# Optimization experiments

Measured on AMD Instinct MI355X. Metric: run time of the kernel, lower is better.

Reference implementation:

```python
import jax, jax.numpy as jnp
import numpy as np

IOU_THRESH = 0.5


def _conv(x, w, b):
    y = jax.lax.conv_general_dilated(
        x, w, window_strides=(1, 1), padding='SAME',
        dimension_numbers=('NCHW', 'OIHW', 'NCHW'))
    return jax.nn.relu(y + b[None, :, None, None])


def _nms_keep(boxes):
    # boxes: [N,4] xyxy, sorted by descending score. Returns bool keep mask [N].
    x1, y1, x2, y2 = boxes[:, 0], boxes[:, 1], boxes[:, 2], boxes[:, 3]
    area = jnp.maximum(x2 - x1, 0.0) * jnp.maximum(y2 - y1, 0.0)
    xx1 = jnp.maximum(x1[:, None], x1[None, :])
    yy1 = jnp.maximum(y1[:, None], y1[None, :])
    xx2 = jnp.minimum(x2[:, None], x2[None, :])
    yy2 = jnp.minimum(y2[:, None], y2[None, :])
    inter = jnp.maximum(xx2 - xx1, 0.0) * jnp.maximum(yy2 - yy1, 0.0)
    iou = inter / (area[:, None] + area[None, :] - inter + 1e-9)  # [N,N]
    n = boxes.shape[0]
    idx = jnp.arange(n)

    def body(i, keep):
        # suppress later boxes that overlap box i too much, if i itself is kept
        suppress = (iou[i] > IOU_THRESH) & (idx > i) & keep[i]
        return keep & ~suppress

    return jax.lax.fori_loop(0, n, body, jnp.ones((n,), dtype=bool))


def setup_inputs() -> dict:
    key = jax.random.key(0)
    k = jax.random.split(key, 7)
    B, N = 32, 100
    x = jax.random.normal(k[0], (B, 3, 224, 224), dtype=jnp.float32)
    boxes = jax.random.uniform(k[1], (B, N, 4), dtype=jnp.float32) * 224.0
    scores = jax.random.uniform(k[2], (B, N), dtype=jnp.float32)
    w1 = jax.random.normal(k[3], (64, 3, 3, 3), dtype=jnp.float32) * (1.0 / np.sqrt(3 * 9))
    b1 = jnp.zeros((64,), dtype=jnp.float32)
    w2 = jax.random.normal(k[4], (128, 64, 3, 3), dtype=jnp.float32) * (1.0 / np.sqrt(64 * 9))
    b2 = jnp.zeros((128,), dtype=jnp.float32)
    return {'x': x, 'boxes': boxes, 'scores': scores,
            'w1': w1, 'b1': b1, 'w2': w2, 'b2': b2}


def reference(x, boxes, scores, w1, b1, w2, b2):
    # backbone: conv-relu-conv-relu-globalavgpool-flatten -> [B,128]
    h = _conv(x, w1, b1)
    h = _conv(h, w2, b2)
    feats = jnp.mean(h, axis=(2, 3))  # AdaptiveAvgPool2d((1,1)) + Flatten

    # per-image sort by descending score
    order = jnp.argsort(-scores, axis=1)                         # [B,N]
    boxes_sorted = jnp.take_along_axis(boxes, order[..., None], axis=1)
    scores_sorted = jnp.take_along_axis(scores, order, axis=1)

    # batched greedy NMS; fixed-shape keep mask instead of ragged index lists
    keep = jax.vmap(_nms_keep)(boxes_sorted)                     # [B,N] bool

    final_boxes = jnp.where(keep[..., None], boxes_sorted, 0.0)
    final_scores = jnp.where(keep, scores_sorted, 0.0)
    return feats, final_boxes, final_scores, keep
```

## Files before the change

### kernel.cpp

```cpp
#include <hip/hip_runtime.h>
#include <hip/hip_bf16.h>

#define HH 224
#define WW 224

#define OUT_FEATS  0
#define OUT_BOXES  4096
#define OUT_SCORES 16896
#define OUT_KEEP   20096

typedef __attribute__((ext_vector_type(8))) short short8;
typedef __attribute__((ext_vector_type(4))) float f32x4;
typedef __attribute__((ext_vector_type(4))) unsigned int u32x4;
typedef __attribute__((ext_vector_type(2))) unsigned int u32x2;

static __device__ __forceinline__ unsigned short f2bf(float f) {
    __hip_bfloat16 h = __float2bfloat16(f);
    return *(unsigned short*)&h;
}

static __device__ __forceinline__ void gload_lds16(const void* g, void* l) {
    __builtin_amdgcn_global_load_lds(
        (const __attribute__((address_space(1))) unsigned int*)g,
        (__attribute__((address_space(3))) unsigned int*)l, 16, 0, 0);
}

__global__ void w2_convert(const float* __restrict__ w2, unsigned short* __restrict__ w2bf)
{
    int t = blockIdx.x * 256 + threadIdx.x;
    if (t >= 9 * 128 * 64) return;
    int tap = t >> 13;
    int rem = t & 8191;
    int oc = rem >> 6, ic = rem & 63;
    w2bf[t] = f2bf(w2[(oc * 64 + ic) * 9 + tap]);
}

__global__ void w1_convert(const float* __restrict__ w1, unsigned short* __restrict__ w1bf)
{
    int t = blockIdx.x * 256 + threadIdx.x;
    if (t >= 64 * 32) return;
    int oc = t >> 5, k = t & 31;
    unsigned short v = 0;
    if (k < 27) v = f2bf(w1[oc * 27 + k]);
    w1bf[t] = v;
}

__global__ __launch_bounds__(256) void fused_conv_kernel(const float* __restrict__ x,
                                                         const unsigned short* __restrict__ w1bf,
                                                         const float* __restrict__ b1,
                                                         const unsigned short* __restrict__ w2bf,
                                                         const float* __restrict__ b2,
                                                         float* __restrict__ partial)
{
    const int xt = blockIdx.x, yt = blockIdx.y, b = blockIdx.z;
    const int x0 = xt * 16, ty0 = yt * 8;
    const int tid = threadIdx.x;
    const int w = tid >> 6, lane = tid & 63;
    const int wm = w >> 1, wn = w & 1;
    const int l15 = lane & 15, lq = lane >> 4;

    __shared__ char smem[43136];
    short* halo   = (short*)smem;
    char*  wlds   = smem + 23040;
    float* xpatch = (float*)(smem + 39424);

    int stage_src[4], stage_dst[4];
#pragma unroll
    for (int it = 0; it < 4; ++it) {
        int cbase = it * 256 + w * 64;
        int c = cbase + lane;
        stage_src[it] = (c * 16) ^ (((c >> 3) & 7) << 4);
        stage_dst[it] = cbase * 16;
    }

#pragma unroll
    for (int it = 0; it < 4; ++it)
        gload_lds16((const char*)w2bf + stage_src[it], wlds + stage_dst[it]);

    for (int i = tid; i < 928; i += 256) {
        float v = 0.f;
        if (i < 720) {
            int ic = i / 240; int rem = i - ic * 240;
            int r = rem / 20, c = rem - r * 20;
            int gy = ty0 - 2 + r, gx = x0 - 2 + c;
            if (gy >= 0 && gy < HH && gx >= 0 && gx < WW)
                v = x[((b * 3 + ic) * HH + gy) * WW + gx];
        }
        xpatch[i] = v;
    }

    short8 aw[4];
#pragma unroll
    for (int f = 0; f < 4; f++)
        aw[f] = *(const short8*)(w1bf + (f * 16 + l15) * 32 + lq * 8);
    float bias1[4][4];
#pragma unroll
    for (int f = 0; f < 4; f++)
#pragma unroll
        for (int j = 0; j < 4; j++)
            bias1[f][j] = b1[f * 16 + lq * 4 + j];

    int koff[8];
#pragma unroll
    for (int j = 0; j < 8; j++) {
        int k = lq * 8 + j;
        int ic = (k >= 18) ? 2 : (k >= 9 ? 1 : 0);
        int t = k - ic * 9;
        int dy = (t >= 6) ? 2 : (t >= 3 ? 1 : 0);
        int dx = t - dy * 3;
        koff[j] = (k < 27) ? ((ic * 12 + dy) * 20 + dx) * 4 : 2880;
    }
    __syncthreads();

    const char* xpb = (const char*)xpatch;
    for (int g = w; g < 12; g += 4) {
        int px0 = g * 16 + l15;
        int px = px0 > 179 ? 179 : px0;
        int row = (px * 456) >> 13;
        int col = px - row * 18;
        int rofs = row * 80 + col * 4;

        float pv[8];
#pragma unroll
        for (int j = 0; j < 8; j++)
            pv[j] = *(const float*)(xpb + (koff[j] + rofs));
        short8 bp;
        unsigned int* bpu = (unsigned int*)&bp;
#pragma unroll
        for (int jj = 0; jj < 4; jj++)
            bpu[jj] = (unsigned int)f2bf(pv[2 * jj]) | ((unsigned int)f2bf(pv[2 * jj + 1]) << 16);

        int gy = ty0 + row - 1, gx = x0 + col - 1;
        float vm = (gy >= 0 && gy < HH && gx >= 0 && gx < WW) ? 1.f : 0.f;
        bool wr = (px0 < 180);

#pragma unroll
        for (int f = 0; f < 4; f++) {
            f32x4 c = __builtin_amdgcn_mfma_f32_16x16x32_bf16(aw[f], bp,
                        (f32x4){0.f, 0.f, 0.f, 0.f}, 0, 0, 0);
            float v0 = fmaxf(c[0] + bias1[f][0], 0.f) * vm;
            float v1 = fmaxf(c[1] + bias1[f][1], 0.f) * vm;
            float v2 = fmaxf(c[2] + bias1[f][2], 0.f) * vm;
            float v3 = fmaxf(c[3] + bias1[f][3], 0.f) * vm;
            if (wr) {
                u32x2 pk;
                pk.x = (unsigned int)f2bf(v0) | ((unsigned int)f2bf(v1) << 16);
                pk.y = (unsigned int)f2bf(v2) | ((unsigned int)f2bf(v3) << 16);
                int byte = (px * 128 + f * 32 + lq * 8) ^ ((px & 7) << 4);
                *(u32x2*)((char*)halo + byte) = pk;
            }
        }
    }

    int a_addr[6][3][2];
#pragma unroll
    for (int rr = 0; rr < 6; rr++)
#pragma unroll
        for (int dx = 0; dx < 3; dx++)
#pragma unroll
            for (int kk = 0; kk < 2; kk++) {
                int pos = (wm * 4 + rr) * 18 + l15 + dx;
                a_addr[rr][dx][kk] = (pos * 128 + kk * 64 + lq * 16) ^ ((pos & 7) << 4);
            }
    int b_addr[4][2];
#pragma unroll
    for (int nf = 0; nf < 4; nf++)
#pragma unroll
        for (int kk = 0; kk < 2; kk++) {
            int oc = wn * 64 + nf * 16 + l15;
            b_addr[nf][kk] = (oc * 128 + kk * 64 + lq * 16) ^ ((oc & 7) << 4);
        }
    __syncthreads();

    f32x4 acc[4][4];
#pragma unroll
    for (int mf = 0; mf < 4; mf++)
#pragma unroll
        for (int nf = 0; nf < 4; nf++)
            acc[mf][nf] = (f32x4){0.f, 0.f, 0.f, 0.f};

#pragma unroll
    for (int t = 0; t < 9; ++t) {
        const int dy = t / 3, dx = t % 3;
#pragma unroll
        for (int kk = 0; kk < 2; kk++) {
            short8 bfr[4];
#pragma unroll
            for (int nf = 0; nf < 4; nf++)
                bfr[nf] = *(const short8*)(wlds + b_addr[nf][kk]);
            short8 a[4];
#pragma unroll
            for (int mf = 0; mf < 4; mf++)
                a[mf] = *(const short8*)((const char*)halo + a_addr[mf + dy][dx][kk]);
#pragma unroll
            for (int mf = 0; mf < 4; mf++)
#pragma unroll
                for (int nf = 0; nf < 4; nf++)
                    acc[mf][nf] = __builtin_amdgcn_mfma_f32_16x16x32_bf16(a[mf], bfr[nf], acc[mf][nf], 0, 0, 0);
        }
        __syncthreads();
        if (t < 8) {
            const char* wsrc = (const char*)w2bf + (t + 1) * 16384;
#pragma unroll
            for (int it = 0; it < 4; ++it)
                gload_lds16(wsrc + stage_src[it], wlds + stage_dst[it]);
            __syncthreads();
        }
    }

    float s[4];
#pragma unroll
    for (int nf = 0; nf < 4; nf++) {
        float bias = b2[wn * 64 + nf * 16 + l15];
        float v = 0.f;
#pragma unroll
        for (int mf = 0; mf < 4; mf++)
#pragma unroll
            for (int j = 0; j < 4; j++)
                v += fmaxf(acc[mf][nf][j] + bias, 0.f);
        v += __shfl_xor(v, 16, 64);
        v += __shfl_xor(v, 32, 64);
        s[nf] = v;
    }

    float* red = (float*)halo;
    if (lq == 0) {
#pragma unroll
        for (int nf = 0; nf < 4; nf++)
            red[((wm * 2 + wn) * 4 + nf) * 16 + l15] = s[nf];
    }
    __syncthreads();
    if (tid < 128) {
        int oc = tid;
        int wn2 = oc >> 6, nf2 = (oc >> 4) & 3, c16 = oc & 15;
        float tot = red[((0 * 2 + wn2) * 4 + nf2) * 16 + c16] +
                    red[((1 * 2 + wn2) * 4 + nf2) * 16 + c16];
        int tile = yt * 14 + xt;
        partial[((size_t)b * 128 + oc) * 392 + tile] = tot;
    }
}

__global__ void feats_reduce(const float* __restrict__ partial, float* __restrict__ out)
{
    int t = blockIdx.x;
    int lane = threadIdx.x;
    float s = 0.f;
    for (int k = lane; k < 392; k += 64) s += partial[(size_t)t * 392 + k];
#pragma unroll
    for (int m = 32; m >= 1; m >>= 1) s += __shfl_xor(s, m, 64);
    if (lane == 0) out[t] = s * (1.f / 50176.f);
}

__global__ __launch_bounds__(128) void nms_kernel(const float* __restrict__ boxes,
                                                  const float* __restrict__ scores,
                                                  float* __restrict__ out)
{
    const int b = blockIdx.x;
    const int tid = threadIdx.x;
    __shared__ float rs[100];
    __shared__ float bx1[100], by1[100], bx2[100], by2[100];
    __shared__ float ss[100], sx1[100], sy1[100], sx2[100], sy2[100], sarea[100];
    __shared__ int keep_s[100];

    if (tid < 100) {
        rs[tid] = scores[b * 100 + tid];
        bx1[tid] = boxes[(b * 100 + tid) * 4 + 0];
        by1[tid] = boxes[(b * 100 + tid) * 4 + 1];
        bx2[tid] = boxes[(b * 100 + tid) * 4 + 2];
        by2[tid] = boxes[(b * 100 + tid) * 4 + 3];
    }
    __syncthreads();
    if (tid < 100) {
        float s = rs[tid];
        int r = 0;
        for (int j = 0; j < 100; j++) {
            float sj = rs[j];
            r += (sj > s) || (sj == s && j < tid);
        }
        ss[r] = s; sx1[r] = bx1[tid]; sy1[r] = by1[tid];
        sx2[r] = bx2[tid]; sy2[r] = by2[tid];
        keep_s[tid] = 1;
    }
    __syncthreads();
    if (tid < 100)
        sarea[tid] = fmaxf(sx2[tid] - sx1[tid], 0.f) * fmaxf(sy2[tid] - sy1[tid], 0.f);
    __syncthreads();

    for (int i = 0; i < 99; i++) {
        if (keep_s[i] && tid > i && tid < 100) {
            float xx1 = fmaxf(sx1[i], sx1[tid]);
            float yy1 = fmaxf(sy1[i], sy1[tid]);
            float xx2 = fminf(sx2[i], sx2[tid]);
            float yy2 = fminf(sy2[i], sy2[tid]);
            float inter = fmaxf(xx2 - xx1, 0.f) * fmaxf(yy2 - yy1, 0.f);
            float iou = inter / (sarea[i] + sarea[tid] - inter + 1e-9f);
            if (iou > 0.5f) keep_s[tid] = 0;
        }
        __syncthreads();
    }

    if (tid < 100) {
        int k = keep_s[tid];
        int gi = b * 100 + tid;
        out[OUT_BOXES + gi * 4 + 0] = k ? sx1[tid] : 0.f;
        out[OUT_BOXES + gi * 4 + 1] = k ? sy1[tid] : 0.f;
        out[OUT_BOXES + gi * 4 + 2] = k ? sx2[tid] : 0.f;
        out[OUT_BOXES + gi * 4 + 3] = k ? sy2[tid] : 0.f;
        out[OUT_SCORES + gi] = k ? ss[tid] : 0.f;
        out[OUT_KEEP + gi] = k ? 1.f : 0.f;
    }
}

extern "C" void kernel_launch(void* const* d_in, const int* in_sizes, int n_in,
                              void* d_out, int out_size, void* d_ws, size_t ws_size,
                              hipStream_t stream)
{
    const float* x      = (const float*)d_in[0];
    const float* boxes  = (const float*)d_in[1];
    const float* scores = (const float*)d_in[2];
    const float* w1     = (const float*)d_in[3];
    const float* b1     = (const float*)d_in[4];
    const float* w2     = (const float*)d_in[5];
    const float* b2     = (const float*)d_in[6];
    float* out = (float*)d_out;

    char* wsb = (char*)d_ws;
    unsigned short* w2bf = (unsigned short*)wsb;
    unsigned short* w1bf = (unsigned short*)(wsb + 9 * 128 * 64 * 2);
    float*          partial = (float*)(wsb + 9 * 128 * 64 * 2 + 64 * 32 * 2);

    w2_convert<<<(9 * 128 * 64 + 255) / 256, 256, 0, stream>>>(w2, w2bf);
    w1_convert<<<8, 256, 0, stream>>>(w1, w1bf);

    fused_conv_kernel<<<dim3(14, 28, 32), 256, 0, stream>>>(x, w1bf, b1, w2bf, b2, partial);

    feats_reduce<<<4096, 64, 0, stream>>>(partial, out + OUT_FEATS);
    nms_kernel<<<32, 128, 0, stream>>>(boxes, scores, out);
}
```

Baseline: 312.4 us.

## Pipeline conv2 weight staging through a four-slot LDS ring with half-tap granularity

The conv2 weight loads are now split into 18 half-tap chunks and staged two steps ahead into a 4-slot LDS ring, with the swizzle layout adjusted to fit. This replaces the per-tap sync, load, sync sequence that stalled the MFMAs. Each step uses explicit vmcnt waits plus a single barrier, and MFMA issue priority is raised with s_setprio. LDS use grows from about 43 KB to 59.5 KB, which may lower occupancy, and the hand-written waitcnt logic is fragile.

```diff
diff --git a/kernel.cpp b/kernel.cpp
--- a/kernel.cpp
+++ b/kernel.cpp
@@ -59,23 +59,19 @@
     const int wm = w >> 1, wn = w & 1;
     const int l15 = lane & 15, lq = lane >> 4;
 
-    __shared__ char smem[43136];
+    __shared__ char smem[59520];
     short* halo   = (short*)smem;
-    char*  wlds   = smem + 23040;
-    float* xpatch = (float*)(smem + 39424);
-
-    int stage_src[4], stage_dst[4];
-#pragma unroll
-    for (int it = 0; it < 4; ++it) {
-        int cbase = it * 256 + w * 64;
-        int c = cbase + lane;
-        stage_src[it] = (c * 16) ^ (((c >> 3) & 7) << 4);
-        stage_dst[it] = cbase * 16;
-    }
-
-#pragma unroll
-    for (int it = 0; it < 4; ++it)
-        gload_lds16((const char*)w2bf + stage_src[it], wlds + stage_dst[it]);
+    char*  slots  = smem + 23040;
+    float* xpatch = (float*)(smem + 55808);
+
+    const int oc0 = tid >> 2, m0 = tid & 3;
+    const int src0 = oc0 * 128 + ((m0 ^ (oc0 & 3)) << 4);
+    const int dst0 = tid << 4;
+
+    gload_lds16((const char*)w2bf + src0,        slots + dst0);
+    gload_lds16((const char*)w2bf + src0 + 8192, slots + dst0 + 4096);
+    gload_lds16((const char*)w2bf + 64 + src0,        slots + 8192 + dst0);
+    gload_lds16((const char*)w2bf + 64 + src0 + 8192, slots + 8192 + dst0 + 4096);
 
     for (int i = tid; i < 928; i += 256) {
         float v = 0.f;
@@ -162,14 +158,12 @@
                 int pos = (wm * 4 + rr) * 18 + l15 + dx;
                 a_addr[rr][dx][kk] = (pos * 128 + kk * 64 + lq * 16) ^ ((pos & 7) << 4);
             }
-    int b_addr[4][2];
-#pragma unroll
-    for (int nf = 0; nf < 4; nf++)
-#pragma unroll
-        for (int kk = 0; kk < 2; kk++) {
-            int oc = wn * 64 + nf * 16 + l15;
-            b_addr[nf][kk] = (oc * 128 + kk * 64 + lq * 16) ^ ((oc & 7) << 4);
-        }
+    int b_addr[4];
+#pragma unroll
+    for (int nf = 0; nf < 4; nf++) {
+        int oc = wn * 64 + nf * 16 + l15;
+        b_addr[nf] = oc * 64 + ((lq ^ (l15 & 3)) << 4);
+    }
     __syncthreads();
 
     f32x4 acc[4][4];
@@ -180,32 +174,41 @@
             acc[mf][nf] = (f32x4){0.f, 0.f, 0.f, 0.f};
 
 #pragma unroll
-    for (int t = 0; t < 9; ++t) {
+    for (int p = 0; p < 18; ++p) {
+        const int t = p >> 1, kk = p & 1;
         const int dy = t / 3, dx = t % 3;
-#pragma unroll
-        for (int kk = 0; kk < 2; kk++) {
-            short8 bfr[4];
+
+        if (p < 16) {
+            const int ps = p + 2;
+            const char* wsrc = (const char*)w2bf + (ps >> 1) * 16384 + (ps & 1) * 64;
+            char* wdst = slots + (ps & 3) * 8192 + dst0;
+            gload_lds16(wsrc + src0, wdst);
+            gload_lds16(wsrc + src0 + 8192, wdst + 4096);
+        }
+
+        if (p < 16)      asm volatile("s_waitcnt vmcnt(4) lgkmcnt(0)" ::: "memory");
+        else if (p == 16) asm volatile("s_waitcnt vmcnt(2) lgkmcnt(0)" ::: "memory");
+        else              asm volatile("s_waitcnt vmcnt(0) lgkmcnt(0)" ::: "memory");
+        __builtin_amdgcn_s_barrier();
+        asm volatile("" ::: "memory");
+
+        const char* wbuf = slots + (p & 3) * 8192;
+        short8 bfr[4];
+#pragma unroll
+        for (int nf = 0; nf < 4; nf++)
+            bfr[nf] = *(const short8*)(wbuf + b_addr[nf]);
+        short8 a[4];
+#pragma unroll
+        for (int mf = 0; mf < 4; mf++)
+            a[mf] = *(const short8*)((const char*)halo + a_addr[mf + dy][dx][kk]);
+
+        __builtin_amdgcn_s_setprio(1);
+#pragma unroll
+        for (int mf = 0; mf < 4; mf++)
 #pragma unroll
             for (int nf = 0; nf < 4; nf++)
-                bfr[nf] = *(const short8*)(wlds + b_addr[nf][kk]);
-            short8 a[4];
-#pragma unroll
-            for (int mf = 0; mf < 4; mf++)
-                a[mf] = *(const short8*)((const char*)halo + a_addr[mf + dy][dx][kk]);
-#pragma unroll
-            for (int mf = 0; mf < 4; mf++)
-#pragma unroll
-                for (int nf = 0; nf < 4; nf++)
-                    acc[mf][nf] = __builtin_amdgcn_mfma_f32_16x16x32_bf16(a[mf], bfr[nf], acc[mf][nf], 0, 0, 0);
-        }
-        __syncthreads();
-        if (t < 8) {
-            const char* wsrc = (const char*)w2bf + (t + 1) * 16384;
-#pragma unroll
-            for (int it = 0; it < 4; ++it)
-                gload_lds16(wsrc + stage_src[it], wlds + stage_dst[it]);
-            __syncthreads();
-        }
+                acc[mf][nf] = __builtin_amdgcn_mfma_f32_16x16x32_bf16(a[mf], bfr[nf], acc[mf][nf], 0, 0, 0);
+        __builtin_amdgcn_s_setprio(0);
     }
 
     float s[4];
@@ -223,6 +226,7 @@
         s[nf] = v;
     }
 
+    __syncthreads();
     float* red = (float*)halo;
     if (lq == 0) {
 #pragma unroll
```

Measured after the change: 318.5 us. About the same (+1.9%).

## Enlarge conv tile to 32 rows and split output channels across blocks

Applied to the files above, without the earlier changes.

The fused conv kernel now handles a 32x16 spatial tile per block, using 512 threads with eight waves each covering four rows. Output channels are split into two halves across blocks. All nine w2 taps for that half are preloaded into LDS once, which removes the per-tap reload and its barriers. The larger tile cuts redundant halo recompute of conv1 along y, but conv1 is now computed twice, once per channel half. It also uses about 157 KB of LDS per block, which limits occupancy to one block per CU.

```diff
diff --git a/kernel.cpp b/kernel.cpp
--- a/kernel.cpp
+++ b/kernel.cpp
@@ -45,47 +45,44 @@
     w1bf[t] = v;
 }
 
-__global__ __launch_bounds__(256) void fused_conv_kernel(const float* __restrict__ x,
+__global__ __launch_bounds__(512) void fused_conv_kernel(const float* __restrict__ x,
                                                          const unsigned short* __restrict__ w1bf,
                                                          const float* __restrict__ b1,
                                                          const unsigned short* __restrict__ w2bf,
                                                          const float* __restrict__ b2,
                                                          float* __restrict__ partial)
 {
-    const int xt = blockIdx.x, yt = blockIdx.y, b = blockIdx.z;
-    const int x0 = xt * 16, ty0 = yt * 8;
+    const int bx = blockIdx.x;
+    const int xt = bx % 14, och = bx / 14;
+    const int yt = blockIdx.y, b = blockIdx.z;
+    const int x0 = xt * 16, ty0 = yt * 32;
     const int tid = threadIdx.x;
     const int w = tid >> 6, lane = tid & 63;
-    const int wm = w >> 1, wn = w & 1;
     const int l15 = lane & 15, lq = lane >> 4;
 
-    __shared__ char smem[43136];
+    __shared__ char smem[160704];
     short* halo   = (short*)smem;
-    char*  wlds   = smem + 23040;
-    float* xpatch = (float*)(smem + 39424);
-
-    int stage_src[4], stage_dst[4];
-#pragma unroll
-    for (int it = 0; it < 4; ++it) {
-        int cbase = it * 256 + w * 64;
-        int c = cbase + lane;
-        stage_src[it] = (c * 16) ^ (((c >> 3) & 7) << 4);
-        stage_dst[it] = cbase * 16;
-    }
-
-#pragma unroll
-    for (int it = 0; it < 4; ++it)
-        gload_lds16((const char*)w2bf + stage_src[it], wlds + stage_dst[it]);
-
-    for (int i = tid; i < 928; i += 256) {
+    char*  wlds   = smem + 78336;
+    float* xpatch = (float*)(smem + 152064);
+
+    {
+        const char* wsrc = (const char*)w2bf + och * 8192;
+#pragma unroll
+        for (int it = 0; it < 9; ++it) {
+            int c = tid + it * 512;
+            int tap = c >> 9, r = c & 511;
+            int src = tap * 16384 + ((r * 16) ^ (((r >> 3) & 7) << 4));
+            gload_lds16(wsrc + src, (char*)wlds + c * 16);
+        }
+    }
+
+    for (int i = tid; i < 2160; i += 512) {
+        int ic = i / 720; int rem = i - ic * 720;
+        int r = rem / 20, c = rem - r * 20;
+        int gy = ty0 - 2 + r, gx = x0 - 2 + c;
         float v = 0.f;
-        if (i < 720) {
-            int ic = i / 240; int rem = i - ic * 240;
-            int r = rem / 20, c = rem - r * 20;
-            int gy = ty0 - 2 + r, gx = x0 - 2 + c;
-            if (gy >= 0 && gy < HH && gx >= 0 && gx < WW)
-                v = x[((b * 3 + ic) * HH + gy) * WW + gx];
-        }
+        if (gy >= 0 && gy < HH && gx >= 0 && gx < WW)
+            v = x[((b * 3 + ic) * HH + gy) * WW + gx];
         xpatch[i] = v;
     }
 
@@ -108,15 +105,15 @@
         int t = k - ic * 9;
         int dy = (t >= 6) ? 2 : (t >= 3 ? 1 : 0);
         int dx = t - dy * 3;
-        koff[j] = (k < 27) ? ((ic * 12 + dy) * 20 + dx) * 4 : 2880;
+        koff[j] = (k < 27) ? ((ic * 36 + dy) * 20 + dx) * 4 : 0;
     }
     __syncthreads();
 
     const char* xpb = (const char*)xpatch;
-    for (int g = w; g < 12; g += 4) {
+    for (int g = w; g < 39; g += 8) {
         int px0 = g * 16 + l15;
-        int px = px0 > 179 ? 179 : px0;
-        int row = (px * 456) >> 13;
+        int px = px0 > 611 ? 611 : px0;
+        int row = (px * 7282) >> 17;
         int col = px - row * 18;
         int rofs = row * 80 + col * 4;
 
@@ -132,7 +129,7 @@
 
         int gy = ty0 + row - 1, gx = x0 + col - 1;
         float vm = (gy >= 0 && gy < HH && gx >= 0 && gx < WW) ? 1.f : 0.f;
-        bool wr = (px0 < 180);
+        bool wr = (px0 < 612);
 
 #pragma unroll
         for (int f = 0; f < 4; f++) {
@@ -159,7 +156,7 @@
         for (int dx = 0; dx < 3; dx++)
 #pragma unroll
             for (int kk = 0; kk < 2; kk++) {
-                int pos = (wm * 4 + rr) * 18 + l15 + dx;
+                int pos = (w * 4 + rr) * 18 + l15 + dx;
                 a_addr[rr][dx][kk] = (pos * 128 + kk * 64 + lq * 16) ^ ((pos & 7) << 4);
             }
     int b_addr[4][2];
@@ -167,7 +164,7 @@
     for (int nf = 0; nf < 4; nf++)
 #pragma unroll
         for (int kk = 0; kk < 2; kk++) {
-            int oc = wn * 64 + nf * 16 + l15;
+            int oc = nf * 16 + l15;
             b_addr[nf][kk] = (oc * 128 + kk * 64 + lq * 16) ^ ((oc & 7) << 4);
         }
     __syncthreads();
@@ -182,12 +179,13 @@
 #pragma unroll
     for (int t = 0; t < 9; ++t) {
         const int dy = t / 3, dx = t % 3;
+        const char* wbuf = (const char*)wlds + t * 8192;
 #pragma unroll
         for (int kk = 0; kk < 2; kk++) {
             short8 bfr[4];
 #pragma unroll
             for (int nf = 0; nf < 4; nf++)
-                bfr[nf] = *(const short8*)(wlds + b_addr[nf][kk]);
+                bfr[nf] = *(const short8*)(wbuf + b_addr[nf][kk]);
             short8 a[4];
 #pragma unroll
             for (int mf = 0; mf < 4; mf++)
@@ -198,20 +196,12 @@
                 for (int nf = 0; nf < 4; nf++)
                     acc[mf][nf] = __builtin_amdgcn_mfma_f32_16x16x32_bf16(a[mf], bfr[nf], acc[mf][nf], 0, 0, 0);
         }
-        __syncthreads();
-        if (t < 8) {
-            const char* wsrc = (const char*)w2bf + (t + 1) * 16384;
-#pragma unroll
-            for (int it = 0; it < 4; ++it)
-                gload_lds16(wsrc + stage_src[it], wlds + stage_dst[it]);
-            __syncthreads();
-        }
     }
 
     float s[4];
 #pragma unroll
     for (int nf = 0; nf < 4; nf++) {
-        float bias = b2[wn * 64 + nf * 16 + l15];
+        float bias = b2[och * 64 + nf * 16 + l15];
         float v = 0.f;
 #pragma unroll
         for (int mf = 0; mf < 4; mf++)
@@ -223,20 +213,22 @@
         s[nf] = v;
     }
 
-    float* red = (float*)halo;
+    float* red = (float*)(smem + 152064);
     if (lq == 0) {
 #pragma unroll
         for (int nf = 0; nf < 4; nf++)
-            red[((wm * 2 + wn) * 4 + nf) * 16 + l15] = s[nf];
-    }
-    __syncthreads();
-    if (tid < 128) {
-        int oc = tid;
-        int wn2 = oc >> 6, nf2 = (oc >> 4) & 3, c16 = oc & 15;
-        float tot = red[((0 * 2 + wn2) * 4 + nf2) * 16 + c16] +
-                    red[((1 * 2 + wn2) * 4 + nf2) * 16 + c16];
+            red[(w * 4 + nf) * 16 + l15] = s[nf];
+    }
+    __syncthreads();
+    if (tid < 64) {
+        int oc_l = tid;
+        int nf2 = oc_l >> 4, c16 = oc_l & 15;
+        float tot = 0.f;
+#pragma unroll
+        for (int ww = 0; ww < 8; ww++)
+            tot += red[(ww * 4 + nf2) * 16 + c16];
         int tile = yt * 14 + xt;
-        partial[((size_t)b * 128 + oc) * 392 + tile] = tot;
+        partial[((size_t)b * 128 + och * 64 + oc_l) * 98 + tile] = tot;
     }
 }
 
@@ -245,7 +237,7 @@
     int t = blockIdx.x;
     int lane = threadIdx.x;
     float s = 0.f;
-    for (int k = lane; k < 392; k += 64) s += partial[(size_t)t * 392 + k];
+    for (int k = lane; k < 98; k += 64) s += partial[(size_t)t * 98 + k];
 #pragma unroll
     for (int m = 32; m >= 1; m >>= 1) s += __shfl_xor(s, m, 64);
     if (lane == 0) out[t] = s * (1.f / 50176.f);
@@ -332,7 +324,7 @@
     w2_convert<<<(9 * 128 * 64 + 255) / 256, 256, 0, stream>>>(w2, w2bf);
     w1_convert<<<8, 256, 0, stream>>>(w1, w1bf);
 
-    fused_conv_kernel<<<dim3(14, 28, 32), 256, 0, stream>>>(x, w1bf, b1, w2bf, b2, partial);
+    fused_conv_kernel<<<dim3(28, 7, 32), 512, 0, stream>>>(x, w1bf, b1, w2bf, b2, partial);
 
     feats_reduce<<<4096, 64, 0, stream>>>(partial, out + OUT_FEATS);
     nms_kernel<<<32, 128, 0, stream>>>(boxes, scores, out);
```

Measured after the change: 312.4 us. Within noise of the previous version (+0.0%).
